# Optimization experiments

Hardware: AMD Instinct MI355X
Metric: run time of the kernel (lower is better)

Reference implementation:

```python
import jax, jax.numpy as jnp
import numpy as np
from jax import lax

STRIDES = (32, 16, 8)
NC = 80
REG_MAX = 16
OFFSET = 0.5


def _conv(x, w, b, pad):
    # NCHW conv, OIHW weight
    y = lax.conv_general_dilated(x, w, (1, 1), [(pad, pad), (pad, pad)],
                                 dimension_numbers=('NCHW', 'OIHW', 'NCHW'))
    return y + b[None, :, None, None]


def _gen_anchors(shapes):
    pts, st = [], []
    for (h, w), s in zip(shapes, STRIDES):
        xx, yy = jnp.meshgrid(jnp.arange(w, dtype=jnp.float32) + OFFSET,
                              jnp.arange(h, dtype=jnp.float32) + OFFSET, indexing='xy')
        pts.append(jnp.stack([xx, yy], axis=-1).reshape(-1, 2))
        st.append(jnp.full((h * w, 1), float(s), jnp.float32))
    return jnp.concatenate(pts, 0), jnp.concatenate(st, 0)


def _level(feat, p):
    cfw, cfb, ccw, ccb, rfw, rfb, rcw, rcb, pcw, pcb, prw, prb = p
    b, _, h, w = feat.shape
    avg = jnp.mean(feat, axis=(2, 3), keepdims=True)  # adaptive_avg_pool2d to 1x1
    # cls branch: ESEAttn gate + 1x1 ConvBNAct(SiLU, BN folded), residual add, 3x3 pred
    wc = jax.nn.sigmoid(_conv(avg, cfw, cfb, 0))
    sc = jax.nn.silu(_conv(feat * wc, ccw, ccb, 0))
    cls_logit = _conv(sc + feat, pcw, pcb, 1)
    # reg branch
    wr = jax.nn.sigmoid(_conv(avg, rfw, rfb, 0))
    sr = jax.nn.silu(_conv(feat * wr, rcw, rcb, 0))
    reg = _conv(sr, prw, prb, 1).reshape(b, 4, REG_MAX + 1, h * w)
    # DFL integral decode: softmax over 17 bins, dot with proj = [0..16]
    proj = jnp.arange(REG_MAX + 1, dtype=jnp.float32)
    dist = jnp.einsum('bakn,k->bna', jax.nn.softmax(reg, axis=2), proj)  # [b, hw, 4]
    cls = jax.nn.sigmoid(cls_logit).reshape(b, NC, h * w)
    return cls, dist


def setup_inputs() -> dict:
    chans = (768, 384, 192)
    sizes = ((20, 20), (40, 40), (80, 80))
    bsz = 16
    keys = iter(jax.random.split(jax.random.key(0), 128))
    inp = {}
    for i, (c, (h, w)) in enumerate(zip(chans, sizes)):
        inp[f'feat{i}'] = jax.random.normal(next(keys), (bsz, c, h, w), jnp.float32)
        for pre in ('cf', 'rf'):
            inp[f'{pre}_w{i}'] = jax.random.normal(next(keys), (c, c, 1, 1), jnp.float32) * 0.001
            inp[f'{pre}_b{i}'] = jnp.zeros((c,), jnp.float32)
        for pre in ('cc', 'rc'):
            inp[f'{pre}_w{i}'] = jax.random.normal(next(keys), (c, c, 1, 1), jnp.float32) * 0.02
            inp[f'{pre}_b{i}'] = jnp.zeros((c,), jnp.float32)
        inp[f'pc_w{i}'] = jax.random.normal(next(keys), (NC, c, 3, 3), jnp.float32) * 0.01
        inp[f'pc_b{i}'] = jnp.full((NC,), float(-np.log(99.0)), jnp.float32)  # bias_init_with_prob(0.01)
        inp[f'pr_w{i}'] = jax.random.normal(next(keys), (4 * (REG_MAX + 1), c, 3, 3), jnp.float32) * 0.01
        inp[f'pr_b{i}'] = jnp.ones((4 * (REG_MAX + 1),), jnp.float32)
    return inp


def reference(feat0, cf_w0, cf_b0, rf_w0, rf_b0, cc_w0, cc_b0, rc_w0, rc_b0, pc_w0, pc_b0, pr_w0, pr_b0,
              feat1, cf_w1, cf_b1, rf_w1, rf_b1, cc_w1, cc_b1, rc_w1, rc_b1, pc_w1, pc_b1, pr_w1, pr_b1,
              feat2, cf_w2, cf_b2, rf_w2, rf_b2, cc_w2, cc_b2, rc_w2, rc_b2, pc_w2, pc_b2, pr_w2, pr_b2):
    feats = [feat0, feat1, feat2]
    params = [
        (cf_w0, cf_b0, cc_w0, cc_b0, rf_w0, rf_b0, rc_w0, rc_b0, pc_w0, pc_b0, pr_w0, pr_b0),
        (cf_w1, cf_b1, cc_w1, cc_b1, rf_w1, rf_b1, rc_w1, rc_b1, pc_w1, pc_b1, pr_w1, pr_b1),
        (cf_w2, cf_b2, cc_w2, cc_b2, rf_w2, rf_b2, rc_w2, rc_b2, pc_w2, pc_b2, pr_w2, pr_b2),
    ]
    cls_l, reg_l, shapes = [], [], []
    for f, p in zip(feats, params):
        c, d = _level(f, p)
        cls_l.append(c)
        reg_l.append(d)
        shapes.append((f.shape[2], f.shape[3]))
    cls_all = jnp.concatenate(cls_l, axis=-1)   # [b, NC, 8400]
    reg_all = jnp.concatenate(reg_l, axis=1)    # [b, 8400, 4]
    anchor_points, stride_tensor = _gen_anchors(shapes)
    return cls_all, reg_all, anchor_points, stride_tensor
```

## Files before the change

kernel.cpp:

```cpp
#include <hip/hip_runtime.h>
#include <hip/hip_bf16.h>

typedef __attribute__((ext_vector_type(8))) short bf16x8;
typedef __attribute__((ext_vector_type(4))) float f32x4;
typedef __attribute__((ext_vector_type(4))) unsigned short u16x4;
typedef unsigned short u16;
typedef unsigned int u32;

#define BSZ 16
#define RO 10752000
#define AO 11289600
#define SO 11306400

__device__ __forceinline__ float sigm(float x) { return 1.f / (1.f + __expf(-x)); }

__device__ __forceinline__ u16 f2bf(float f) {
  u32 u = __float_as_uint(f);
  u = u + 0x7FFF + ((u >> 16) & 1);
  return (u16)(u >> 16);
}
__device__ __forceinline__ float bf2f(u16 v) { return __uint_as_float(((u32)v) << 16); }

__device__ __forceinline__ void gll16(const void* g, void* l) {
  __builtin_amdgcn_global_load_lds((const __attribute__((address_space(1))) void*)g,
                                   (__attribute__((address_space(3))) void*)l, 16, 0, 0);
}

__device__ __forceinline__ int xswz(int bid, int n) {
  int q = n >> 3, r = n & 7;
  int x = bid & 7, i = bid >> 3;
  return (x < r ? x * (q + 1) : r * (q + 1) + (x - r) * q) + i;
}

__global__ __launch_bounds__(256) void k_anchor(float* out) {
  int g = blockIdx.x * 256 + threadIdx.x;
  if (g >= 8400) return;
  int l = g < 400 ? 0 : (g < 2000 ? 1 : 2);
  int off = l == 0 ? 0 : (l == 1 ? 400 : 2000);
  int w = 20 << l;
  float s = (float)(32 >> l);
  int p = g - off;
  int x = p % w, y = p / w;
  out[AO + 2 * g] = x + 0.5f;
  out[AO + 2 * g + 1] = y + 0.5f;
  out[SO + g] = s;
}

struct PFArgs { const float* feat[3]; u16* fT[3]; float* avg; };

__global__ __launch_bounds__(256) void k_prepF2(PFArgs A, int s1, int s2) {
  __shared__ float buf[32][65];
  int bid = blockIdx.x;
  int l = bid >= s2 ? 2 : (bid >= s1 ? 1 : 0);
  int loc = bid - (l == 2 ? s2 : (l == 1 ? s1 : 0));
  int C = 768 >> l, HW = 400 << (2 * l);
  int PT = (HW + 63) / 64;
  int pt = loc % PT, b = loc / PT;
  int p0 = pt * 64;
  int tid = threadIdx.x;
  int cc = tid >> 6, pp = tid & 63;
  int pload = p0 + pp;
  bool lok = pload < HW;
  int plc = lok ? pload : 0;
  int pw = tid >> 2, cg = (tid & 3) * 8;
  bool wok = p0 + pw < HW;
  int rch = tid >> 3, rgp = tid & 7;
  const float* src = A.feat[l] + (size_t)b * C * HW;
  u16* dst = A.fT[l] + (size_t)b * HW * C;
  float* avgb = A.avg + (l * BSZ + b) * 768;
  for (int c0 = 0; c0 < C; c0 += 32) {
#pragma unroll
    for (int j = 0; j < 8; j++) {
      int c = c0 + cc * 8 + j;
      float v = src[(size_t)c * HW + plc];
      buf[cc * 8 + j][pp] = lok ? v : 0.f;
    }
    __syncthreads();
    if (wok) {
      bf16x8 h;
#pragma unroll
      for (int j = 0; j < 8; j++) h[j] = (short)f2bf(buf[cg + j][pw]);
      *(bf16x8*)(dst + (size_t)(p0 + pw) * C + c0 + cg) = h;
    }
    {
      float v = 0.f;
#pragma unroll
      for (int k = 0; k < 8; k++) v += buf[rch][rgp * 8 + k];
      v += __shfl_xor(v, 1);
      v += __shfl_xor(v, 2);
      v += __shfl_xor(v, 4);
      if (rgp == 0) atomicAdd(avgb + c0 + rch, v);
    }
    __syncthreads();
  }
}

struct GArgs {
  const float *cfw[3], *cfb[3], *rfw[3], *rfb[3];
  float *avg, *gc, *gr;
};

__global__ __launch_bounds__(256) void k_gate(GArgs A, int s1, int s2) {
  int bid = blockIdx.x;
  int l = bid >= s2 ? 2 : (bid >= s1 ? 1 : 0);
  int loc = bid - (l == 2 ? s2 : (l == 1 ? s1 : 0));
  int C = 768 >> l, HW = 400 << (2 * l);
  float inv = 1.f / (float)HW;
  int co = loc % C, b = loc / C;
  const float* av = A.avg + (l * BSZ + b) * 768;
  float sc = 0.f, sr = 0.f;
  for (int ci = threadIdx.x; ci < C; ci += 256) {
    float v = av[ci];
    sc += A.cfw[l][(size_t)co * C + ci] * v;
    sr += A.rfw[l][(size_t)co * C + ci] * v;
  }
  __shared__ float rc[256], rr[256];
  rc[threadIdx.x] = sc; rr[threadIdx.x] = sr;
  __syncthreads();
  for (int o = 128; o > 0; o >>= 1) {
    if (threadIdx.x < o) { rc[threadIdx.x] += rc[threadIdx.x + o]; rr[threadIdx.x] += rr[threadIdx.x + o]; }
    __syncthreads();
  }
  if (threadIdx.x == 0) {
    A.gc[(l * BSZ + b) * 768 + co] = sigm(rc[0] * inv + A.cfb[l][co]);
    A.gr[(l * BSZ + b) * 768 + co] = sigm(rr[0] * inv + A.rfb[l][co]);
  }
}

struct GWArgs {
  const float *w0[3], *w1[3];
  const float *gc, *gr;
  u16 *gwc, *gwr;
  long goff[3];
};

__global__ __launch_bounds__(256) void k_wgate(GWArgs A, int s1, int s2) {
  int bid = blockIdx.x;
  int l = bid >= s2 ? 2 : (bid >= s1 ? 1 : 0);
  int loc = bid - (l == 2 ? s2 : (l == 1 ? s1 : 0));
  int C = 768 >> l;
  int per_b = (C * C) >> 11;
  int tile = loc % per_b, b = loc / per_b;
  int idx = (tile << 11) + threadIdx.x * 8;
  int co = idx / C, ci = idx - co * C;
  const float* g0 = A.gc + (l * BSZ + b) * 768 + ci;
  const float* g1 = A.gr + (l * BSZ + b) * 768 + ci;
  const float* w0 = A.w0[l] + idx;
  const float* w1 = A.w1[l] + idx;
  f32x4 wa0 = *(const f32x4*)(w0), wb0 = *(const f32x4*)(w0 + 4);
  f32x4 wa1 = *(const f32x4*)(w1), wb1 = *(const f32x4*)(w1 + 4);
  f32x4 ga = *(const f32x4*)(g0), gb = *(const f32x4*)(g0 + 4);
  f32x4 ra = *(const f32x4*)(g1), rb = *(const f32x4*)(g1 + 4);
  bf16x8 h0, h1;
#pragma unroll
  for (int j = 0; j < 4; j++) {
    h0[j] = (short)f2bf(wa0[j] * ga[j]);
    h0[j + 4] = (short)f2bf(wb0[j] * gb[j]);
    h1[j] = (short)f2bf(wa1[j] * ra[j]);
    h1[j + 4] = (short)f2bf(wb1[j] * rb[j]);
  }
  size_t o = A.goff[l] + (size_t)b * C * C + idx;
  *(bf16x8*)(A.gwc + o) = h0;
  *(bf16x8*)(A.gwr + o) = h1;
}

__global__ __launch_bounds__(256) void k_wprep(const float* w, u16* dst, int C) {
  int id = blockIdx.x * 256 + threadIdx.x;
  int co = id / C, ci = id - co * C;
  const float* s = w + (size_t)id * 9;
#pragma unroll
  for (int t = 0; t < 9; t++) dst[((size_t)(t * 96 + co)) * C + ci] = f2bf(s[t]);
}

struct C1WLvl {
  const u16 *gwc, *gwr;
  const float *b0, *b1;
  const u16* fT;
  u16 *tcT, *trT;
  int C, HW, ntiles, mblks, bstart, cnt;
};
struct C1WArgs { C1WLvl l[3]; };

__global__ __launch_bounds__(256) void k_conv1p(C1WArgs A) {
  __shared__ char smem[65536];
  int bid = blockIdx.x;
  int li = (bid >= A.l[2].bstart) ? 2 : (bid >= A.l[1].bstart ? 1 : 0);
  const C1WLvl& L = A.l[li];
  int loc = xswz(bid - L.bstart, L.cnt);
  int mb = loc % L.mblks;
  int t2 = loc / L.mblks;
  int nt = t2 % L.ntiles;
  int b = t2 / L.ntiles;
  const int C = L.C, HW = L.HW;
  int p0 = nt * 128, co0 = mb * 64;
  int tid = threadIdx.x, lane = tid & 63, w = tid >> 6;
  int wm = w >> 1, wn = w & 1;
  const u16* fTb = L.fT + (size_t)b * HW * C;
  const u16* gw0 = L.gwc + (size_t)b * C * C;
  const u16* gw1 = L.gwr + (size_t)b * C * C;
  int sl8 = lane & 7;

  const u16* bsrc[4];
#pragma unroll
  for (int i = 0; i < 4; i++) {
    int r = w * 32 + i * 8 + (lane >> 3);
    int p = p0 + r;
    if (p >= HW) p = HW - 1;
    bsrc[i] = fTb + (size_t)p * C + ((sl8 ^ (r & 7)) << 3);
  }
  const u16 *a0src[2], *a1src[2];
#pragma unroll
  for (int i = 0; i < 2; i++) {
    int r = w * 16 + i * 8 + (lane >> 3);
    a0src[i] = gw0 + (size_t)(co0 + r) * C + ((sl8 ^ (r & 7)) << 3);
    a1src[i] = gw1 + (size_t)(co0 + r) * C + ((sl8 ^ (r & 7)) << 3);
  }
  int aoff[2][2], boff[2][4];
#pragma unroll
  for (int ks = 0; ks < 2; ks++) {
    int sl = ks * 4 + (lane >> 4);
#pragma unroll
    for (int mi = 0; mi < 2; mi++) {
      int ar = wm * 32 + mi * 16 + (lane & 15);
      aoff[ks][mi] = ar * 128 + ((sl ^ (ar & 7)) << 4);
    }
#pragma unroll
    for (int ni = 0; ni < 4; ni++) {
      int br = wn * 64 + ni * 16 + (lane & 15);
      boff[ks][ni] = br * 128 + ((sl ^ (br & 7)) << 4);
    }
  }

  f32x4 acc0[2][4], acc1[2][4];
#pragma unroll
  for (int mi = 0; mi < 2; mi++)
#pragma unroll
    for (int ni = 0; ni < 4; ni++) { acc0[mi][ni] = (f32x4){0.f,0.f,0.f,0.f}; acc1[mi][ni] = (f32x4){0.f,0.f,0.f,0.f}; }

  const int nchunk = C >> 6;
  {
    char* buf = smem;
#pragma unroll
    for (int i = 0; i < 4; i++) gll16(bsrc[i], buf + 16384 + (w * 32 + i * 8) * 128);
#pragma unroll
    for (int i = 0; i < 2; i++) {
      gll16(a0src[i], buf + (w * 16 + i * 8) * 128);
      gll16(a1src[i], buf + 8192 + (w * 16 + i * 8) * 128);
    }
  }

  int cur = 0;
  for (int c = 0; c < nchunk; c++) {
    if (c + 1 < nchunk) {
      int cb = (c + 1) << 6;
      char* buf = smem + ((cur ^ 1) << 15);
#pragma unroll
      for (int i = 0; i < 4; i++) gll16(bsrc[i] + cb, buf + 16384 + (w * 32 + i * 8) * 128);
#pragma unroll
      for (int i = 0; i < 2; i++) {
        gll16(a0src[i] + cb, buf + (w * 16 + i * 8) * 128);
        gll16(a1src[i] + cb, buf + 8192 + (w * 16 + i * 8) * 128);
      }
      asm volatile("s_waitcnt vmcnt(8)" ::: "memory");
    } else {
      asm volatile("s_waitcnt vmcnt(0)" ::: "memory");
    }
    __builtin_amdgcn_sched_barrier(0);
    __builtin_amdgcn_s_barrier();
    __builtin_amdgcn_sched_barrier(0);

    char* B0 = smem + (cur << 15);
#pragma unroll
    for (int ks = 0; ks < 2; ks++) {
      bf16x8 a0[2], a1[2], bf[4];
#pragma unroll
      for (int mi = 0; mi < 2; mi++) {
        a0[mi] = *(const bf16x8*)(B0 + aoff[ks][mi]);
        a1[mi] = *(const bf16x8*)(B0 + 8192 + aoff[ks][mi]);
      }
#pragma unroll
      for (int ni = 0; ni < 4; ni++) bf[ni] = *(const bf16x8*)(B0 + 16384 + boff[ks][ni]);
#pragma unroll
      for (int mi = 0; mi < 2; mi++)
#pragma unroll
        for (int ni = 0; ni < 4; ni++) {
          acc0[mi][ni] = __builtin_amdgcn_mfma_f32_16x16x32_bf16(a0[mi], bf[ni], acc0[mi][ni], 0, 0, 0);
          acc1[mi][ni] = __builtin_amdgcn_mfma_f32_16x16x32_bf16(a1[mi], bf[ni], acc1[mi][ni], 0, 0, 0);
        }
    }
    __builtin_amdgcn_sched_barrier(0);
    __builtin_amdgcn_s_barrier();
    __builtin_amdgcn_sched_barrier(0);
    cur ^= 1;
  }

#pragma unroll
  for (int mi = 0; mi < 2; mi++) {
    int cob = co0 + wm * 32 + mi * 16 + ((lane >> 4) << 2);
    f32x4 bia0 = *(const f32x4*)(L.b0 + cob);
    f32x4 bia1 = *(const f32x4*)(L.b1 + cob);
#pragma unroll
    for (int ni = 0; ni < 4; ni++) {
      int p = p0 + wn * 64 + ni * 16 + (lane & 15);
      if (p >= HW) continue;
      u16x4 res = *(const u16x4*)(fTb + (size_t)p * C + cob);
      u16x4 o0, o1;
#pragma unroll
      for (int j = 0; j < 4; j++) {
        float x0 = acc0[mi][ni][j] + bia0[j];
        o0[j] = f2bf(x0 * sigm(x0) + bf2f(res[j]));
        float x1 = acc1[mi][ni][j] + bia1[j];
        o1[j] = f2bf(x1 * sigm(x1));
      }
      size_t off = ((size_t)b * HW + p) * C + cob;
      *(u16x4*)(L.tcT + off) = o0;
      *(u16x4*)(L.trT + off) = o1;
    }
  }
}

struct C3Lvl {
  const u16* inT;
  const u16* wT;
  const float* bias;
  int C, W, H, HW, ntiles, bstart, pos_off;
};
struct C3MArgs { C3Lvl lc[3]; C3Lvl lr[3]; const u16* zp; float* out; int half; };

__global__ __launch_bounds__(256) void k_conv3m(C3MArgs A) {
  __shared__ char smem[57344];
  int rb = blockIdx.x;
  bool isReg = rb >= A.half;
  int bid = isReg ? rb - A.half : rb;
  const C3Lvl* lv = isReg ? A.lr : A.lc;
  int li = (bid >= lv[2].bstart) ? 2 : (bid >= lv[1].bstart ? 1 : 0);
  const C3Lvl& L = lv[li];
  int loc = bid - L.bstart;
  int nt = loc % L.ntiles;
  int b = loc / L.ntiles;
  const int C = L.C, W = L.W, H = L.H, HW = L.HW;
  int p0 = nt * 128;
  int tid = threadIdx.x, lane = tid & 63, w = tid >> 6;
  int wm = w >> 1, wn = w & 1;
  int sl8 = lane & 7;
  const u16* inb = L.inT + (size_t)b * HW * C;

  int px[4], py[4];
  bool pv[4];
  const u16* bbase[4];
#pragma unroll
  for (int i = 0; i < 4; i++) {
    int r = w * 32 + i * 8 + (lane >> 3);
    int p = p0 + r;
    pv[i] = p < HW;
    int pp = pv[i] ? p : 0;
    px[i] = pp % W;
    py[i] = pp / W;
    bbase[i] = inb + (size_t)pp * C + ((sl8 ^ (r & 7)) << 3);
  }
  const u16* awbase[3];
#pragma unroll
  for (int g = 0; g < 3; g++) {
    int row = w * 24 + g * 8 + (lane >> 3);
    awbase[g] = L.wT + (size_t)row * C + ((sl8 ^ (row & 7)) << 3);
  }
  int aoff[2][3], boff[2][4];
#pragma unroll
  for (int ks = 0; ks < 2; ks++) {
    int sl = ks * 4 + (lane >> 4);
#pragma unroll
    for (int mi = 0; mi < 3; mi++) {
      int ar = wm * 48 + mi * 16 + (lane & 15);
      aoff[ks][mi] = ar * 128 + ((sl ^ (ar & 7)) << 4);
    }
#pragma unroll
    for (int ni = 0; ni < 4; ni++) {
      int br = wn * 64 + ni * 16 + (lane & 15);
      boff[ks][ni] = br * 128 + ((sl ^ (br & 7)) << 4);
    }
  }

  f32x4 acc[3][4];
#pragma unroll
  for (int mi = 0; mi < 3; mi++)
#pragma unroll
    for (int ni = 0; ni < 4; ni++) acc[mi][ni] = (f32x4){0.f,0.f,0.f,0.f};

  const int nchunk = C >> 6;
  const int total = 9 * nchunk;

  auto STAGE = [&](int t, int cb, char* buf) {
    int dy = t / 3 - 1, dx = t - (t / 3) * 3 - 1;
    long shift = (long)(dy * W + dx) * C;
    size_t ash = (size_t)t * 96 * C + cb;
#pragma unroll
    for (int g = 0; g < 3; g++) gll16(awbase[g] + ash, buf + (w * 24 + g * 8) * 128);
#pragma unroll
    for (int i = 0; i < 4; i++) {
      int xx = px[i] + dx, yy = py[i] + dy;
      bool ok = pv[i] && ((unsigned)xx < (unsigned)W) && ((unsigned)yy < (unsigned)H);
      const void* src = ok ? (const void*)(bbase[i] + shift + cb) : (const void*)A.zp;
      gll16(src, buf + 12288 + (w * 32 + i * 8) * 128);
    }
  };

  STAGE(0, 0, smem);

  int cur = 0, t = 0, c = 0;
  for (int s = 0; s < total; s++) {
    int tn = t + 1, cn = c;
    if (tn == 9) { tn = 0; cn = c + 1; }
    if (s + 1 < total) {
      STAGE(tn, cn << 6, smem + ((cur ^ 1) * 28672));
      asm volatile("s_waitcnt vmcnt(7)" ::: "memory");
    } else {
      asm volatile("s_waitcnt vmcnt(0)" ::: "memory");
    }
    __builtin_amdgcn_sched_barrier(0);
    __builtin_amdgcn_s_barrier();
    __builtin_amdgcn_sched_barrier(0);

    char* B0 = smem + cur * 28672;
#pragma unroll
    for (int ks = 0; ks < 2; ks++) {
      bf16x8 af[3], bf[4];
#pragma unroll
      for (int mi = 0; mi < 3; mi++) af[mi] = *(const bf16x8*)(B0 + aoff[ks][mi]);
#pragma unroll
      for (int ni = 0; ni < 4; ni++) bf[ni] = *(const bf16x8*)(B0 + 12288 + boff[ks][ni]);
#pragma unroll
      for (int mi = 0; mi < 3; mi++)
#pragma unroll
        for (int ni = 0; ni < 4; ni++)
          acc[mi][ni] = __builtin_amdgcn_mfma_f32_16x16x32_bf16(af[mi], bf[ni], acc[mi][ni], 0, 0, 0);
    }
    __builtin_amdgcn_sched_barrier(0);
    __builtin_amdgcn_s_barrier();
    __builtin_amdgcn_sched_barrier(0);
    cur ^= 1; t = tn; c = cn;
  }

  if (!isReg) {
#pragma unroll
    for (int mi = 0; mi < 3; mi++) {
      int cob = wm * 48 + mi * 16 + ((lane >> 4) << 2);
      if (cob >= 80) continue;
      f32x4 bia = *(const f32x4*)(L.bias + cob);
#pragma unroll
      for (int ni = 0; ni < 4; ni++) {
        int p = p0 + wn * 64 + ni * 16 + (lane & 15);
        if (p >= HW) continue;
#pragma unroll
        for (int j = 0; j < 4; j++)
          A.out[(size_t)(b * 80 + cob + j) * 8400 + L.pos_off + p] = sigm(acc[mi][ni][j] + bia[j]);
      }
    }
  } else {
    float* P = (float*)smem;
#pragma unroll
    for (int mi = 0; mi < 3; mi++) {
      int cob = wm * 48 + mi * 16 + ((lane >> 4) << 2);
      if (cob < 68) {
        f32x4 bia = *(const f32x4*)(L.bias + cob);
#pragma unroll
        for (int ni = 0; ni < 4; ni++) {
          int n = wn * 64 + ni * 16 + (lane & 15);
          f32x4 v = acc[mi][ni];
#pragma unroll
          for (int j = 0; j < 4; j++) v[j] += bia[j];
          *(f32x4*)(P + n * 68 + cob) = v;
        }
      }
    }
    __syncthreads();
    int n = tid >> 1, g2 = tid & 1;
    int p = p0 + n;
    if (p < HW) {
      float d[2];
#pragma unroll
      for (int gg = 0; gg < 2; gg++) {
        const float* row = P + n * 68 + (g2 * 2 + gg) * 17;
        float mx = row[0];
#pragma unroll
        for (int k = 1; k < 17; k++) mx = fmaxf(mx, row[k]);
        float sum = 0.f, dot = 0.f;
#pragma unroll
        for (int k = 0; k < 17; k++) {
          float e = __expf(row[k] - mx);
          sum += e;
          dot += (float)k * e;
        }
        d[gg] = dot / sum;
      }
      *(float2*)(A.out + RO + ((size_t)b * 8400 + L.pos_off + p) * 4 + g2 * 2) = make_float2(d[0], d[1]);
    }
  }
}

extern "C" void kernel_launch(void* const* d_in, const int* in_sizes, int n_in,
                              void* d_out, int out_size, void* d_ws, size_t ws_size,
                              hipStream_t stream) {
  static const int Cs[3] = {768, 384, 192};
  static const int HWs[3] = {400, 1600, 6400};
  static const int Ws[3] = {20, 40, 80};
  static const int POs[3] = {0, 400, 2000};
  static const long TOFF[3] = {0, 4915200, 14745600};
  static const long WTOFF[3] = {0, 663552, 995328};
  static const long GOFF[3] = {0, 9437184, 11796480};
  static const int NT[3] = {4, 13, 50};
  static const int MB[3] = {12, 6, 3};

  char* wsb = (char*)d_ws;
  u16* zp = (u16*)wsb;
  float* avg = (float*)(wsb + 256);
  float* gc = avg + 3 * BSZ * 768;
  float* gr = gc + 3 * BSZ * 768;
  u16* tcT = (u16*)(gr + 3 * BSZ * 768);
  u16* trT = tcT + 34406400;
  u16* wTc = trT + 34406400;
  u16* wTr = wTc + 1161216;
  u16* featT = wTr + 1161216;
  u16* gwc = featT + 34406400;
  u16* gwr = gwc + 12386304;

  hipMemsetAsync(zp, 0, 256, stream);
  hipMemsetAsync(avg, 0, 3 * BSZ * 768 * sizeof(float), stream);
  hipMemsetAsync(wTc, 0, 2 * 1161216ull * 2, stream);

  for (int l = 0; l < 3; l++) {
    const float* pcw = (const float*)d_in[l * 13 + 9];
    const float* prw = (const float*)d_in[l * 13 + 11];
    hipLaunchKernelGGL(k_wprep, dim3(80 * Cs[l] / 256), dim3(256), 0, stream, pcw, wTc + WTOFF[l], Cs[l]);
    hipLaunchKernelGGL(k_wprep, dim3(68 * Cs[l] / 256), dim3(256), 0, stream, prw, wTr + WTOFF[l], Cs[l]);
  }

  {
    PFArgs PF;
    for (int l = 0; l < 3; l++) {
      PF.feat[l] = (const float*)d_in[l * 13 + 0];
      PF.fT[l] = featT + TOFF[l];
    }
    PF.avg = avg;
    int ps1 = BSZ * 7, ps2 = ps1 + BSZ * 25, ptot = ps2 + BSZ * 100;
    hipLaunchKernelGGL(k_prepF2, dim3(ptot), dim3(256), 0, stream, PF, ps1, ps2);
  }

  {
    GArgs GA;
    for (int l = 0; l < 3; l++) {
      const float* const* p = (const float* const*)(d_in + l * 13);
      GA.cfw[l] = p[1]; GA.cfb[l] = p[2];
      GA.rfw[l] = p[3]; GA.rfb[l] = p[4];
    }
    GA.avg = avg; GA.gc = gc; GA.gr = gr;
    int s1 = BSZ * 768, s2 = s1 + BSZ * 384, tot = s2 + BSZ * 192;
    hipLaunchKernelGGL(k_gate, dim3(tot), dim3(256), 0, stream, GA, s1, s2);
  }

  {
    GWArgs GW;
    for (int l = 0; l < 3; l++) {
      const float* const* p = (const float* const*)(d_in + l * 13);
      GW.w0[l] = p[5];
      GW.w1[l] = p[7];
      GW.goff[l] = GOFF[l];
    }
    GW.gc = gc; GW.gr = gr;
    GW.gwc = gwc; GW.gwr = gwr;
    int g1 = BSZ * 288, g2 = g1 + BSZ * 72, gtot = g2 + BSZ * 18;
    hipLaunchKernelGGL(k_wgate, dim3(gtot), dim3(256), 0, stream, GW, g1, g2);
  }

  {
    C1WArgs C1;
    int bstart = 0;
    for (int l = 0; l < 3; l++) {
      const float* const* p = (const float* const*)(d_in + l * 13);
      C1WLvl& L = C1.l[l];
      L.gwc = gwc + GOFF[l];
      L.gwr = gwr + GOFF[l];
      L.b0 = p[6]; L.b1 = p[8];
      L.fT = featT + TOFF[l];
      L.tcT = tcT + TOFF[l];
      L.trT = trT + TOFF[l];
      L.C = Cs[l]; L.HW = HWs[l]; L.ntiles = NT[l]; L.mblks = MB[l];
      L.bstart = bstart;
      L.cnt = BSZ * NT[l] * MB[l];
      bstart += L.cnt;
    }
    hipLaunchKernelGGL(k_conv1p, dim3(bstart), dim3(256), 0, stream, C1);
  }

  {
    C3MArgs C3;
    int bs3 = 0;
    for (int l = 0; l < 3; l++) {
      const float* const* p = (const float* const*)(d_in + l * 13);
      C3Lvl Lc, Lr;
      Lc.inT = tcT + TOFF[l]; Lc.wT = wTc + WTOFF[l]; Lc.bias = p[10];
      Lr.inT = trT + TOFF[l]; Lr.wT = wTr + WTOFF[l]; Lr.bias = p[12];
      Lc.C = Lr.C = Cs[l]; Lc.W = Lr.W = Ws[l]; Lc.H = Lr.H = Ws[l]; Lc.HW = Lr.HW = HWs[l];
      Lc.ntiles = Lr.ntiles = NT[l];
      Lc.bstart = Lr.bstart = bs3;
      Lc.pos_off = Lr.pos_off = POs[l];
      C3.lc[l] = Lc; C3.lr[l] = Lr;
      bs3 += BSZ * NT[l];
    }
    C3.zp = zp; C3.out = (float*)d_out;
    C3.half = bs3;
    hipLaunchKernelGGL(k_conv3m, dim3(2 * bs3), dim3(256), 0, stream, C3);
  }

  hipLaunchKernelGGL(k_anchor, dim3(33), dim3(256), 0, stream, (float*)d_out);
}
```

Before: 408.1 us.

## Load 3x3 conv weight fragments directly into registers instead of staging through LDS

The weight (A) operand of the 3x3 prediction conv is now fetched from global memory straight into register fragments, double-buffered across two register sets, instead of being staged through LDS with global_load_lds. LDS use per block shrinks to just the double-buffered activation tiles, which may allow more blocks per CU and removes LDS reads for A. The cost is more VGPRs and uncoalesced per-lane 16-byte global loads of weights, with the wait count raised to cover the extra outstanding loads.

Result: slower. 535.4 us (+31.2%).

```diff
diff --git a/kernel.cpp b/kernel.cpp
--- a/kernel.cpp
+++ b/kernel.cpp
@@ -328,7 +328,7 @@
 struct C3MArgs { C3Lvl lc[3]; C3Lvl lr[3]; const u16* zp; float* out; int half; };
 
 __global__ __launch_bounds__(256) void k_conv3m(C3MArgs A) {
-  __shared__ char smem[57344];
+  __shared__ char smem[34816];
   int rb = blockIdx.x;
   bool isReg = rb >= A.half;
   int bid = isReg ? rb - A.half : rb;
@@ -344,6 +344,7 @@
   int wm = w >> 1, wn = w & 1;
   int sl8 = lane & 7;
   const u16* inb = L.inT + (size_t)b * HW * C;
+  const u16* wA = L.wT;
 
   int px[4], py[4];
   bool pv[4];
@@ -358,21 +359,15 @@
     py[i] = pp / W;
     bbase[i] = inb + (size_t)pp * C + ((sl8 ^ (r & 7)) << 3);
   }
-  const u16* awbase[3];
-#pragma unroll
-  for (int g = 0; g < 3; g++) {
-    int row = w * 24 + g * 8 + (lane >> 3);
-    awbase[g] = L.wT + (size_t)row * C + ((sl8 ^ (row & 7)) << 3);
-  }
-  int aoff[2][3], boff[2][4];
+  int arow[3];
+#pragma unroll
+  for (int mi = 0; mi < 3; mi++) arow[mi] = wm * 48 + mi * 16 + (lane & 15);
+  int akof = (lane >> 4) << 3;
+
+  int boff[2][4];
 #pragma unroll
   for (int ks = 0; ks < 2; ks++) {
     int sl = ks * 4 + (lane >> 4);
-#pragma unroll
-    for (int mi = 0; mi < 3; mi++) {
-      int ar = wm * 48 + mi * 16 + (lane & 15);
-      aoff[ks][mi] = ar * 128 + ((sl ^ (ar & 7)) << 4);
-    }
 #pragma unroll
     for (int ni = 0; ni < 4; ni++) {
       int br = wn * 64 + ni * 16 + (lane & 15);
@@ -389,55 +384,66 @@
   const int nchunk = C >> 6;
   const int total = 9 * nchunk;
 
-  auto STAGE = [&](int t, int cb, char* buf) {
+  auto STAGEB = [&](int t, int cb, char* buf) {
     int dy = t / 3 - 1, dx = t - (t / 3) * 3 - 1;
     long shift = (long)(dy * W + dx) * C;
-    size_t ash = (size_t)t * 96 * C + cb;
-#pragma unroll
-    for (int g = 0; g < 3; g++) gll16(awbase[g] + ash, buf + (w * 24 + g * 8) * 128);
 #pragma unroll
     for (int i = 0; i < 4; i++) {
       int xx = px[i] + dx, yy = py[i] + dy;
       bool ok = pv[i] && ((unsigned)xx < (unsigned)W) && ((unsigned)yy < (unsigned)H);
       const void* src = ok ? (const void*)(bbase[i] + shift + cb) : (const void*)A.zp;
-      gll16(src, buf + 12288 + (w * 32 + i * 8) * 128);
+      gll16(src, buf + (w * 32 + i * 8) * 128);
     }
   };
-
-  STAGE(0, 0, smem);
+  auto LOADA = [&](bf16x8 (&dst)[6], int tt, int cb) {
+#pragma unroll
+    for (int ks = 0; ks < 2; ks++)
+#pragma unroll
+      for (int mi = 0; mi < 3; mi++)
+        dst[ks * 3 + mi] = *(const bf16x8*)(wA + (size_t)(tt * 96 + arow[mi]) * C + cb + ks * 32 + akof);
+  };
+
+  bf16x8 aA[6], aB[6];
+  STAGEB(0, 0, smem);
+  LOADA(aA, 0, 0);
 
   int cur = 0, t = 0, c = 0;
-  for (int s = 0; s < total; s++) {
+  auto STEP = [&](bf16x8 (&use)[6], bf16x8 (&pre)[6], int s) {
     int tn = t + 1, cn = c;
     if (tn == 9) { tn = 0; cn = c + 1; }
     if (s + 1 < total) {
-      STAGE(tn, cn << 6, smem + ((cur ^ 1) * 28672));
-      asm volatile("s_waitcnt vmcnt(7)" ::: "memory");
+      STAGEB(tn, cn << 6, smem + ((cur ^ 1) << 14));
+      LOADA(pre, tn, cn << 6);
+      __builtin_amdgcn_sched_barrier(0);
+      asm volatile("s_waitcnt vmcnt(10)" ::: "memory");
     } else {
       asm volatile("s_waitcnt vmcnt(0)" ::: "memory");
     }
     __builtin_amdgcn_sched_barrier(0);
     __builtin_amdgcn_s_barrier();
     __builtin_amdgcn_sched_barrier(0);
-
-    char* B0 = smem + cur * 28672;
+    char* B0 = smem + (cur << 14);
 #pragma unroll
     for (int ks = 0; ks < 2; ks++) {
-      bf16x8 af[3], bf[4];
-#pragma unroll
-      for (int mi = 0; mi < 3; mi++) af[mi] = *(const bf16x8*)(B0 + aoff[ks][mi]);
-#pragma unroll
-      for (int ni = 0; ni < 4; ni++) bf[ni] = *(const bf16x8*)(B0 + 12288 + boff[ks][ni]);
+      bf16x8 bf[4];
+#pragma unroll
+      for (int ni = 0; ni < 4; ni++) bf[ni] = *(const bf16x8*)(B0 + boff[ks][ni]);
 #pragma unroll
       for (int mi = 0; mi < 3; mi++)
 #pragma unroll
         for (int ni = 0; ni < 4; ni++)
-          acc[mi][ni] = __builtin_amdgcn_mfma_f32_16x16x32_bf16(af[mi], bf[ni], acc[mi][ni], 0, 0, 0);
+          acc[mi][ni] = __builtin_amdgcn_mfma_f32_16x16x32_bf16(use[ks * 3 + mi], bf[ni], acc[mi][ni], 0, 0, 0);
     }
     __builtin_amdgcn_sched_barrier(0);
     __builtin_amdgcn_s_barrier();
     __builtin_amdgcn_sched_barrier(0);
     cur ^= 1; t = tn; c = cn;
+  };
+
+  int s = 0;
+  while (true) {
+    STEP(aA, aB, s); if (++s == total) break;
+    STEP(aB, aA, s); if (++s == total) break;
   }
 
   if (!isReg) {
```
